# Optimization experiments

Hardware: AMD Instinct MI355X
Metric: run time of the kernel (lower is better)

## Reference

```python
import jax, jax.numpy as jnp
import numpy as np

HIDDEN = 256
NUM_REGIMES = 4

def setup_inputs() -> dict:
    key = jax.random.key(0)
    ks = jax.random.split(key, 9)
    B, D, A = 65536, 256, 128
    x = jax.random.normal(ks[0], (B, D), dtype=jnp.float32)
    regime = jax.random.randint(ks[1], (B,), 0, NUM_REGIMES).astype(jnp.float32)
    x = x.at[:, -1].set(regime)  # last feature holds the discrete regime id
    s1 = 1.0 / np.sqrt(D)
    s2 = 1.0 / np.sqrt(HIDDEN)
    W1 = jax.random.uniform(ks[2], (D, HIDDEN), jnp.float32, -s1, s1)
    b1 = jax.random.uniform(ks[3], (HIDDEN,), jnp.float32, -s1, s1)
    W2 = jax.random.uniform(ks[4], (HIDDEN, HIDDEN), jnp.float32, -s2, s2)
    b2 = jax.random.uniform(ks[5], (HIDDEN,), jnp.float32, -s2, s2)
    Wh = jax.random.uniform(ks[6], (NUM_REGIMES, HIDDEN, A), jnp.float32, -s2, s2)
    bh = jax.random.uniform(ks[7], (NUM_REGIMES, A), jnp.float32, -s2, s2)
    log_std = jnp.zeros((A,), dtype=jnp.float32)
    return {"x": x, "W1": W1, "b1": b1, "W2": W2, "b2": b2,
            "Wh": Wh, "bh": bh, "log_std": log_std}

def reference(x, W1, b1, W2, b2, Wh, bh, log_std):
    # regime index from last feature column (hard routing)
    regime_idx = x[:, -1].astype(jnp.int32)  # [B]
    # backbone MLP: Linear-ReLU-Linear-ReLU
    h = jax.nn.relu(x @ W1 + b1)
    feats = jax.nn.relu(h @ W2 + b2)  # [B, HIDDEN]
    # compute all 4 regime heads densely, then gather per-sample head output
    raw_all = jnp.einsum('bh,rha->bra', feats, Wh) + bh[None, :, :]  # [B, 4, A]
    raw = jnp.take_along_axis(raw_all, regime_idx[:, None, None], axis=1)[:, 0, :]  # [B, A]
    mean = raw * 0.1
    std = jnp.clip(jnp.exp(log_std), 1e-3, 1.0)
    std = jnp.broadcast_to(std[None, :], mean.shape)
    return mean, std
```

## Files before the change

### kernel.cpp

```cpp
#include <hip/hip_runtime.h>
#include <hip/hip_bf16.h>
#include <cstddef>


typedef unsigned short u16;
typedef unsigned int   u32;

using bf16x8 = __attribute__((ext_vector_type(8))) __bf16;
using f32x4  = __attribute__((ext_vector_type(4))) float;

#define BM      64
#define LDSW    264
#define THREADS 1024

__device__ __forceinline__ u16 f2bf(float f) {
  return __builtin_bit_cast(u16, (__bf16)f);
}

__global__ void prep_weights(const float* __restrict__ W1,
                             const float* __restrict__ W2,
                             const float* __restrict__ Wh,
                             u16* __restrict__ ws) {
  int i = blockIdx.x * 256 + threadIdx.x;
  {
    int j  = i & 7, l = (i >> 3) & 63, kk = (i >> 9) & 7;
    int w  = (i >> 12) & 15;
    int n = w * 16 + (l & 15);
    int k = kk * 32 + ((l >> 4) << 3) + j;
    ws[i]         = f2bf(W1[k * 256 + n]);
    ws[65536 + i] = f2bf(W2[k * 256 + n]);
  }
#pragma unroll
  for (int t = 0; t < 2; ++t) {
    int idx = i + t * 65536;
    int j  = idx & 7, l = (idx >> 3) & 63, kk = (idx >> 9) & 7;
    int nb = (idx >> 12) & 1, w = (idx >> 13) & 15;
    int c = w * 32 + nb * 16 + (l & 15);
    int k = kk * 32 + ((l >> 4) << 3) + j;
    int r = c >> 7, a = c & 127;
    ws[131072 + idx] = f2bf(Wh[(r * 256 + k) * 128 + a]);
  }
}

__device__ __forceinline__ void gemm16(f32x4 acc[4], const u16* A,
                                       const u16* __restrict__ Wp,
                                       int ar, int kg, int lane) {
#pragma unroll
  for (int kk = 0; kk < 8; ++kk) {
    const int k = kk * 32 + kg;
    bf16x8 b = *(const bf16x8*)&Wp[(kk * 64 + lane) * 8];
    bf16x8 a[4];
#pragma unroll
    for (int m = 0; m < 4; ++m)
      a[m] = *(const bf16x8*)&A[(m * 16 + ar) * LDSW + k];
#pragma unroll
    for (int m = 0; m < 4; ++m)
      acc[m] = __builtin_amdgcn_mfma_f32_16x16x32_bf16(a[m], b, acc[m], 0, 0, 0);
  }
}

__device__ __forceinline__ void epilogue_relu(f32x4 acc[4], const float* __restrict__ bias,
                                              u16* O, int col, int orow) {
  const float bv = bias[col];
#pragma unroll
  for (int m = 0; m < 4; ++m) {
#pragma unroll
    for (int j = 0; j < 4; ++j) {
      float v = acc[m][j] + bv;
      v = v > 0.f ? v : 0.f;
      O[(m * 16 + orow + j) * LDSW + col] = f2bf(v);
    }
  }
}

__global__ __launch_bounds__(THREADS, 4) void actor_main(
    const float* __restrict__ x,
    const float* __restrict__ b1, const float* __restrict__ b2,
    const float* __restrict__ bh, const float* __restrict__ log_std,
    const u16* __restrict__ wbf,
    float* __restrict__ out_mean, float* __restrict__ out_std) {
  __shared__ u16 bufA[BM * LDSW];
  __shared__ u16 bufB[BM * LDSW];
  __shared__ int s_regime[BM];

  const int tid  = threadIdx.x;
  const int lane = tid & 63;
  const int wave = tid >> 6;
  const int row0 = blockIdx.x * BM;
  const int ar   = lane & 15;
  const int kg   = (lane >> 4) * 8;
  const int orow = (lane >> 4) * 4;
  const int n0   = wave * 16;

  {
    const float4* xg = (const float4*)(x + (size_t)row0 * 256);
#pragma unroll
    for (int it = 0; it < 4; ++it) {
      const int i = tid + it * THREADS;
      float4 v = xg[i];
      int row = i >> 6, c4 = (i & 63) << 2;
      ushort4 b;
      b.x = f2bf(v.x); b.y = f2bf(v.y); b.z = f2bf(v.z); b.w = f2bf(v.w);
      *(ushort4*)&bufA[row * LDSW + c4] = b;
      if (c4 == 252) s_regime[row] = (int)v.w;
    }
  }

  {
    const int c4 = (tid & 31) << 2;
    float4 s;
    s.x = fminf(fmaxf(expf(log_std[c4 + 0]), 1e-3f), 1.0f);
    s.y = fminf(fmaxf(expf(log_std[c4 + 1]), 1e-3f), 1.0f);
    s.z = fminf(fmaxf(expf(log_std[c4 + 2]), 1e-3f), 1.0f);
    s.w = fminf(fmaxf(expf(log_std[c4 + 3]), 1e-3f), 1.0f);
#pragma unroll
    for (int i = tid; i < BM * 32; i += THREADS) {
      int row = i >> 5;
      *(float4*)&out_std[(size_t)(row0 + row) * 128 + c4] = s;
    }
  }
  __syncthreads();

  {
    f32x4 acc[4] = {};
    gemm16(acc, bufA, wbf + wave * 4096, ar, kg, lane);
    epilogue_relu(acc, b1, bufB, n0 + ar, orow);
  }
  __syncthreads();

  {
    f32x4 acc[4] = {};
    gemm16(acc, bufB, wbf + 65536 + wave * 4096, ar, kg, lane);
    epilogue_relu(acc, b2, bufA, n0 + ar, orow);
  }
  __syncthreads();

  {
    const u16* __restrict__ Wp3 = wbf + 131072 + wave * 8192;
    f32x4 acc[4][2] = {};
#pragma unroll
    for (int kk = 0; kk < 8; ++kk) {
      const int k = kk * 32 + kg;
      bf16x8 a[4], b[2];
#pragma unroll
      for (int nb = 0; nb < 2; ++nb)
        b[nb] = *(const bf16x8*)&Wp3[((nb * 8 + kk) * 64 + lane) * 8];
#pragma unroll
      for (int m = 0; m < 4; ++m)
        a[m] = *(const bf16x8*)&bufA[(m * 16 + ar) * LDSW + k];
#pragma unroll
      for (int m = 0; m < 4; ++m)
#pragma unroll
        for (int nb = 0; nb < 2; ++nb)
          acc[m][nb] = __builtin_amdgcn_mfma_f32_16x16x32_bf16(a[m], b[nb], acc[m][nb], 0, 0, 0);
    }
    const int head = wave >> 2;
    const int c0   = (wave & 3) * 32;
#pragma unroll
    for (int nb = 0; nb < 2; ++nb) {
      const int acol = c0 + nb * 16 + ar;
      const float bhv = bh[head * 128 + acol];
#pragma unroll
      for (int m = 0; m < 4; ++m) {
#pragma unroll
        for (int j = 0; j < 4; ++j) {
          const int row = m * 16 + orow + j;
          if (s_regime[row] == head)
            out_mean[(size_t)(row0 + row) * 128 + acol] = 0.1f * (acc[m][nb][j] + bhv);
        }
      }
    }
  }
}

extern "C" void kernel_launch(void* const* d_in, const int* in_sizes, int n_in,
                              void* d_out, int out_size, void* d_ws, size_t ws_size,
                              hipStream_t stream) {
  const float* x  = (const float*)d_in[0];
  const float* W1 = (const float*)d_in[1];
  const float* b1 = (const float*)d_in[2];
  const float* W2 = (const float*)d_in[3];
  const float* b2 = (const float*)d_in[4];
  const float* Wh = (const float*)d_in[5];
  const float* bh = (const float*)d_in[6];
  const float* ls = (const float*)d_in[7];

  const int B = in_sizes[0] / 256;
  float* out_mean = (float*)d_out;
  float* out_std  = out_mean + (size_t)B * 128;
  u16* wbf = (u16*)d_ws;

  hipLaunchKernelGGL(prep_weights, dim3(256), dim3(256), 0, stream, W1, W2, Wh, wbf);
  hipLaunchKernelGGL(actor_main, dim3(B / BM), dim3(THREADS), 0, stream,
                     x, b1, b2, bh, ls, wbf, out_mean, out_std);
}
```

Before: 70.83 us.

## Swap MFMA operands so weights are A, halve threads, vectorize epilogues

The MFMA operand roles are swapped so weight tiles act as the A operand and activations as B. Each accumulator lane then holds four consecutive output columns, which allows ushort4 LDS stores and float4 global stores for bias, hidden outputs and the mean output. The block shrinks to 512 threads, each wave covering twice the output columns, and the weight prepack layout is changed to match. The regime ids are now read straight from global x instead of shared memory. This is meant to cut per-element store instructions and improve reuse per wave, at the cost of more accumulator registers per thread and fewer waves per block.

```diff
diff --git a/kernel.cpp b/kernel.cpp
--- a/kernel.cpp
+++ b/kernel.cpp
@@ -11,7 +11,7 @@
 
 #define BM      64
 #define LDSW    264
-#define THREADS 1024
+#define THREADS 512
 
 __device__ __forceinline__ u16 f2bf(float f) {
   return __builtin_bit_cast(u16, (__bf16)f);
@@ -24,8 +24,8 @@
   int i = blockIdx.x * 256 + threadIdx.x;
   {
     int j  = i & 7, l = (i >> 3) & 63, kk = (i >> 9) & 7;
-    int w  = (i >> 12) & 15;
-    int n = w * 16 + (l & 15);
+    int nt = (i >> 12) & 1, w = (i >> 13) & 7;
+    int n = w * 32 + nt * 16 + (l & 15);
     int k = kk * 32 + ((l >> 4) << 3) + j;
     ws[i]         = f2bf(W1[k * 256 + n]);
     ws[65536 + i] = f2bf(W2[k * 256 + n]);
@@ -34,41 +34,50 @@
   for (int t = 0; t < 2; ++t) {
     int idx = i + t * 65536;
     int j  = idx & 7, l = (idx >> 3) & 63, kk = (idx >> 9) & 7;
-    int nb = (idx >> 12) & 1, w = (idx >> 13) & 15;
-    int c = w * 32 + nb * 16 + (l & 15);
+    int ct = (idx >> 12) & 3, w = (idx >> 14) & 7;
+    int c = w * 64 + ct * 16 + (l & 15);
     int k = kk * 32 + ((l >> 4) << 3) + j;
-    int r = c >> 7, a = c & 127;
-    ws[131072 + idx] = f2bf(Wh[(r * 256 + k) * 128 + a]);
+    ws[131072 + idx] = f2bf(Wh[(c >> 7) * 32768 + k * 128 + (c & 127)]);
   }
 }
 
-__device__ __forceinline__ void gemm16(f32x4 acc[4], const u16* A,
-                                       const u16* __restrict__ Wp,
-                                       int ar, int kg, int lane) {
+__device__ __forceinline__ f32x4 mfma16(bf16x8 a, bf16x8 b, f32x4 c) {
+  return __builtin_amdgcn_mfma_f32_16x16x32_bf16(a, b, c, 0, 0, 0);
+}
+
+__device__ __forceinline__ void gemm_swapped(const u16* __restrict__ act,
+                                             const u16* __restrict__ Wp,
+                                             const float* __restrict__ bias,
+                                             u16* __restrict__ outbuf,
+                                             int w, int ll, int lh, int lane) {
+  f32x4 acc[2][4] = {};
 #pragma unroll
   for (int kk = 0; kk < 8; ++kk) {
-    const int k = kk * 32 + kg;
-    bf16x8 b = *(const bf16x8*)&Wp[(kk * 64 + lane) * 8];
-    bf16x8 a[4];
+    bf16x8 a[2], b[4];
 #pragma unroll
-    for (int m = 0; m < 4; ++m)
-      a[m] = *(const bf16x8*)&A[(m * 16 + ar) * LDSW + k];
+    for (int nt = 0; nt < 2; ++nt)
+      a[nt] = *(const bf16x8*)&Wp[((nt * 8 + kk) * 64 + lane) * 8];
 #pragma unroll
-    for (int m = 0; m < 4; ++m)
-      acc[m] = __builtin_amdgcn_mfma_f32_16x16x32_bf16(a[m], b, acc[m], 0, 0, 0);
+    for (int bt = 0; bt < 4; ++bt)
+      b[bt] = *(const bf16x8*)&act[(bt * 16 + ll) * LDSW + kk * 32 + lh * 8];
+#pragma unroll
+    for (int nt = 0; nt < 2; ++nt)
+#pragma unroll
+      for (int bt = 0; bt < 4; ++bt)
+        acc[nt][bt] = mfma16(a[nt], b[bt], acc[nt][bt]);
   }
-}
-
-__device__ __forceinline__ void epilogue_relu(f32x4 acc[4], const float* __restrict__ bias,
-                                              u16* O, int col, int orow) {
-  const float bv = bias[col];
 #pragma unroll
-  for (int m = 0; m < 4; ++m) {
+  for (int nt = 0; nt < 2; ++nt) {
+    const int n0 = w * 32 + nt * 16 + lh * 4;
+    const float4 bv = *(const float4*)&bias[n0];
 #pragma unroll
-    for (int j = 0; j < 4; ++j) {
-      float v = acc[m][j] + bv;
-      v = v > 0.f ? v : 0.f;
-      O[(m * 16 + orow + j) * LDSW + col] = f2bf(v);
+    for (int bt = 0; bt < 4; ++bt) {
+      ushort4 o;
+      o.x = f2bf(fmaxf(acc[nt][bt][0] + bv.x, 0.f));
+      o.y = f2bf(fmaxf(acc[nt][bt][1] + bv.y, 0.f));
+      o.z = f2bf(fmaxf(acc[nt][bt][2] + bv.z, 0.f));
+      o.w = f2bf(fmaxf(acc[nt][bt][3] + bv.w, 0.f));
+      *(ushort4*)&outbuf[(bt * 16 + ll) * LDSW + n0] = o;
     }
   }
 }
@@ -79,30 +88,26 @@
     const float* __restrict__ bh, const float* __restrict__ log_std,
     const u16* __restrict__ wbf,
     float* __restrict__ out_mean, float* __restrict__ out_std) {
-  __shared__ u16 bufA[BM * LDSW];
-  __shared__ u16 bufB[BM * LDSW];
-  __shared__ int s_regime[BM];
+  __shared__ u16 bufX[BM * LDSW];
+  __shared__ u16 bufH[BM * LDSW];
 
   const int tid  = threadIdx.x;
   const int lane = tid & 63;
-  const int wave = tid >> 6;
+  const int w    = tid >> 6;
+  const int ll   = lane & 15;
+  const int lh   = lane >> 4;
   const int row0 = blockIdx.x * BM;
-  const int ar   = lane & 15;
-  const int kg   = (lane >> 4) * 8;
-  const int orow = (lane >> 4) * 4;
-  const int n0   = wave * 16;
 
   {
     const float4* xg = (const float4*)(x + (size_t)row0 * 256);
 #pragma unroll
-    for (int it = 0; it < 4; ++it) {
+    for (int it = 0; it < 8; ++it) {
       const int i = tid + it * THREADS;
       float4 v = xg[i];
       int row = i >> 6, c4 = (i & 63) << 2;
       ushort4 b;
       b.x = f2bf(v.x); b.y = f2bf(v.y); b.z = f2bf(v.z); b.w = f2bf(v.w);
-      *(ushort4*)&bufA[row * LDSW + c4] = b;
-      if (c4 == 252) s_regime[row] = (int)v.w;
+      *(ushort4*)&bufX[row * LDSW + c4] = b;
     }
   }
 
@@ -121,52 +126,50 @@
   }
   __syncthreads();
 
-  {
-    f32x4 acc[4] = {};
-    gemm16(acc, bufA, wbf + wave * 4096, ar, kg, lane);
-    epilogue_relu(acc, b1, bufB, n0 + ar, orow);
-  }
+  gemm_swapped(bufX, wbf + w * 8192, b1, bufH, w, ll, lh, lane);
+  __syncthreads();
+
+  gemm_swapped(bufH, wbf + 65536 + w * 8192, b2, bufX, w, ll, lh, lane);
   __syncthreads();
 
   {
-    f32x4 acc[4] = {};
-    gemm16(acc, bufB, wbf + 65536 + wave * 4096, ar, kg, lane);
-    epilogue_relu(acc, b2, bufA, n0 + ar, orow);
-  }
-  __syncthreads();
+    const u16* __restrict__ Wp3 = wbf + 131072 + w * 16384;
 
-  {
-    const u16* __restrict__ Wp3 = wbf + 131072 + wave * 8192;
-    f32x4 acc[4][2] = {};
+    int rg[4];
+#pragma unroll
+    for (int bt = 0; bt < 4; ++bt)
+      rg[bt] = (int)x[(size_t)(row0 + bt * 16 + ll) * 256 + 255];
+
+    f32x4 acc[4][4] = {};
 #pragma unroll
     for (int kk = 0; kk < 8; ++kk) {
-      const int k = kk * 32 + kg;
-      bf16x8 a[4], b[2];
+      bf16x8 b[4];
 #pragma unroll
-      for (int nb = 0; nb < 2; ++nb)
-        b[nb] = *(const bf16x8*)&Wp3[((nb * 8 + kk) * 64 + lane) * 8];
+      for (int bt = 0; bt < 4; ++bt)
+        b[bt] = *(const bf16x8*)&bufX[(bt * 16 + ll) * LDSW + kk * 32 + lh * 8];
 #pragma unroll
-      for (int m = 0; m < 4; ++m)
-        a[m] = *(const bf16x8*)&bufA[(m * 16 + ar) * LDSW + k];
+      for (int ct = 0; ct < 4; ++ct) {
+        bf16x8 a = *(const bf16x8*)&Wp3[((ct * 8 + kk) * 64 + lane) * 8];
 #pragma unroll
-      for (int m = 0; m < 4; ++m)
+        for (int bt = 0; bt < 4; ++bt)
+          acc[ct][bt] = mfma16(a, b[bt], acc[ct][bt]);
+      }
+    }
+    const int head = w >> 1;
 #pragma unroll
-        for (int nb = 0; nb < 2; ++nb)
-          acc[m][nb] = __builtin_amdgcn_mfma_f32_16x16x32_bf16(a[m], b[nb], acc[m][nb], 0, 0, 0);
-    }
-    const int head = wave >> 2;
-    const int c0   = (wave & 3) * 32;
+    for (int ct = 0; ct < 4; ++ct) {
+      const int acol = (w & 1) * 64 + ct * 16 + lh * 4;
+      const float4 bhv = *(const float4*)&bh[head * 128 + acol];
 #pragma unroll
-    for (int nb = 0; nb < 2; ++nb) {
-      const int acol = c0 + nb * 16 + ar;
-      const float bhv = bh[head * 128 + acol];
-#pragma unroll
-      for (int m = 0; m < 4; ++m) {
-#pragma unroll
-        for (int j = 0; j < 4; ++j) {
-          const int row = m * 16 + orow + j;
-          if (s_regime[row] == head)
-            out_mean[(size_t)(row0 + row) * 128 + acol] = 0.1f * (acc[m][nb][j] + bhv);
+      for (int bt = 0; bt < 4; ++bt) {
+        const int brow = bt * 16 + ll;
+        if (rg[bt] == head) {
+          float4 o;
+          o.x = 0.1f * (acc[ct][bt][0] + bhv.x);
+          o.y = 0.1f * (acc[ct][bt][1] + bhv.y);
+          o.z = 0.1f * (acc[ct][bt][2] + bhv.z);
+          o.w = 0.1f * (acc[ct][bt][3] + bhv.w);
+          *(float4*)&out_mean[(size_t)(row0 + brow) * 128 + acol] = o;
         }
       }
     }
```

After: 66.67 us. -5.9%, faster.
